# Performance work log

Hardware: AMD Instinct MI355X
Metric: run time of the kernel (lower is better)

The kernel has to match this reference:

```python
import jax, jax.numpy as jnp
import numpy as np
import math

NUM_HEADS = 4
NUM_GROUPS = 16
EPS = 1e-5


def setup_inputs() -> dict:
    key = jax.random.key(0)
    ks = jax.random.split(key, 4)
    C = 256
    x = jax.random.normal(ks[0], (1, C, 16, 16, 16), dtype=jnp.float32)
    gn_gamma = jnp.ones((C,), dtype=jnp.float32)
    gn_beta = jnp.zeros((C,), dtype=jnp.float32)
    # conv3d 1x1 kernels == plain matrices [out_ch, in_ch]
    w_qkv = jax.random.normal(ks[1], (3 * C, C), dtype=jnp.float32) * (1.0 / math.sqrt(C))
    w_proj = jax.random.normal(ks[2], (C, C), dtype=jnp.float32) * (1.0 / math.sqrt(C))
    b_proj = jnp.zeros((C,), dtype=jnp.float32)
    return {"x": x, "gn_gamma": gn_gamma, "gn_beta": gn_beta,
            "w_qkv": w_qkv, "w_proj": w_proj, "b_proj": b_proj}


def reference(x, gn_gamma, gn_beta, w_qkv, w_proj, b_proj):
    B, C, H, W, D = x.shape
    N = H * W * D
    heads = NUM_HEADS
    d = C // heads

    xf = x.reshape(B, C, N)  # [B, C, N]

    # GroupNorm(16, C) with affine params
    xg = xf.reshape(B, NUM_GROUPS, C // NUM_GROUPS, N)
    mu = jnp.mean(xg, axis=(2, 3), keepdims=True)
    var = jnp.var(xg, axis=(2, 3), keepdims=True)
    xn = ((xg - mu) * jax.lax.rsqrt(var + EPS)).reshape(B, C, N)
    xn = xn * gn_gamma[None, :, None] + gn_beta[None, :, None]

    # 1x1 conv QKV: [B, 3C, N]
    qkv = jnp.einsum('oc,bcn->bon', w_qkv, xn)
    # torch: qkv.reshape(B*heads, 3d, N).chunk(3, dim=1)
    qkv = qkv.reshape(B * heads, 3 * d, N)
    q, k, v = qkv[:, :d], qkv[:, d:2 * d], qkv[:, 2 * d:]

    scale = 1.0 / math.sqrt(math.sqrt(d))
    attn = jnp.einsum('bct,bcs->bts', q * scale, k * scale)  # [B*heads, N, N]
    attn = jax.nn.softmax(attn, axis=-1)
    h = jnp.einsum('bts,bcs->bct', attn, v)  # [B*heads, d, N]

    h = h.reshape(B, C, N)
    out = jnp.einsum('oc,bcn->bon', w_proj, h) + b_proj[None, :, None]
    return (out + xf).reshape(B, C, H, W, D)
```

## Files before the change

kernel.cpp:

```cpp
#include <hip/hip_runtime.h>
#include <math.h>

#define N_TOK 4096
#define C_CH  256
#define SPLITS 4

typedef short bf16x8 __attribute__((ext_vector_type(8)));
typedef float f32x4  __attribute__((ext_vector_type(4)));
typedef unsigned short u16;

__device__ __forceinline__ u16 f2bf(float f) {
    union { float f; unsigned u; } v; v.f = f;
    unsigned r = v.u + 0x7FFF + ((v.u >> 16) & 1);
    return (u16)(r >> 16);
}
__device__ __forceinline__ float bf2f(u16 b) {
    union { unsigned u; float f; } v; v.u = ((unsigned)b) << 16;
    return v.f;
}
__device__ __forceinline__ unsigned packtr(float a, float b) {
    union { float f; unsigned u; } ua, ub; ua.f = a; ub.f = b;
    return __builtin_amdgcn_perm(ub.u, ua.u, 0x07060302u);
}

__global__ __launch_bounds__(256) void prep(const float* __restrict__ wqkv,
                                            const float* __restrict__ wproj,
                                            const float* __restrict__ x,
                                            u16* __restrict__ wq, u16* __restrict__ wp,
                                            float2* __restrict__ part) {
    __shared__ float rs[4], rss[4];
    if (blockIdx.x < 1024) {
        int i = blockIdx.x * 256 + threadIdx.x;
        if (i < 196608) {
            int row = i >> 8;
            float s = ((row % 192) < 64) ? 0.125f : 1.0f;
            wq[i] = f2bf(wqkv[i] * s);
        } else {
            wp[i - 196608] = f2bf(wproj[i - 196608]);
        }
    } else {
        const int b = blockIdx.x - 1024, tid = threadIdx.x;
        const int lane = tid & 63, wave = tid >> 6;
        const float4* xp = (const float4*)x + b * 1024;
        float s = 0.f, ss = 0.f;
#pragma unroll
        for (int k = 0; k < 4; ++k) {
            float4 v = xp[tid + k * 256];
            s  += v.x + v.y + v.z + v.w;
            ss += v.x * v.x + v.y * v.y + v.z * v.z + v.w * v.w;
        }
#pragma unroll
        for (int off = 1; off < 64; off <<= 1) {
            s  += __shfl_xor(s, off, 64);
            ss += __shfl_xor(ss, off, 64);
        }
        if (lane == 0) { rs[wave] = s; rss[wave] = ss; }
        __syncthreads();
        if (tid == 0) part[b] = make_float2(rs[0]+rs[1]+rs[2]+rs[3], rss[0]+rss[1]+rss[2]+rss[3]);
    }
}

__global__ __launch_bounds__(256) void norm_t(const float* __restrict__ x,
                                              const float2* __restrict__ part,
                                              const float* __restrict__ gamma,
                                              const float* __restrict__ beta,
                                              u16* __restrict__ xt) {
    const int tb = blockIdx.x * 64, cb = blockIdx.y * 64;
    const int tid = threadIdx.x;
    __shared__ float T[64][65];
    __shared__ float smu[16], srstd[16];
    if (tid < 16) {
        float s = 0.f, ss = 0.f;
#pragma unroll
        for (int j = 0; j < 16; ++j) { float2 p = part[tid * 16 + j]; s += p.x; ss += p.y; }
        float mu = s / 65536.f;
        float var = ss / 65536.f - mu * mu;
        smu[tid] = mu; srstd[tid] = rsqrtf(var + 1e-5f);
    }
    __syncthreads();
#pragma unroll
    for (int it = 0; it < 16; ++it) {
        int idx = tid + it * 256;
        int c = idx >> 6, t = idx & 63;
        int cg = cb + c;
        T[c][t] = (x[cg * N_TOK + tb + t] - smu[cg >> 4]) * srstd[cg >> 4] * gamma[cg] + beta[cg];
    }
    __syncthreads();
#pragma unroll
    for (int it = 0; it < 16; ++it) {
        int idx = tid + it * 256;
        int t = idx >> 6, c = idx & 63;
        xt[(tb + t) * C_CH + cb + c] = f2bf(T[c][t]);
    }
}

__global__ __launch_bounds__(256) void qkv_gemm(const u16* __restrict__ wq,
                                                const u16* __restrict__ xt,
                                                u16* __restrict__ QT,
                                                u16* __restrict__ KTm,
                                                u16* __restrict__ Vc) {
    const int nb = blockIdx.x * 64;
    const int mo = blockIdx.y * 64 + (threadIdx.x >> 6) * 16;
    const int lane = threadIdx.x & 63;
    const int quad = lane >> 4, low = lane & 15;

    f32x4 acc[4] = {f32x4{0,0,0,0}, f32x4{0,0,0,0}, f32x4{0,0,0,0}, f32x4{0,0,0,0}};
#pragma unroll
    for (int kc = 0; kc < 8; ++kc) {
        bf16x8 af = *(const bf16x8*)(wq + (mo + low) * 256 + kc * 32 + quad * 8);
#pragma unroll
        for (int nt = 0; nt < 4; ++nt) {
            bf16x8 bf_ = *(const bf16x8*)(xt + (nb + nt * 16 + low) * 256 + kc * 32 + quad * 8);
            acc[nt] = __builtin_amdgcn_mfma_f32_16x16x32_bf16(af, bf_, acc[nt], 0, 0, 0);
        }
    }
#pragma unroll
    for (int r = 0; r < 4; ++r) {
        int o = mo + quad * 4 + r;
        int head = o / 192, rem = o % 192, c = rem & 63;
#pragma unroll
        for (int nt = 0; nt < 4; ++nt) {
            int tok = nb + nt * 16 + low;
            u16 v = f2bf(acc[nt][r]);
            if (rem < 64)       QT [(head * N_TOK + tok) * 64 + c] = v;
            else if (rem < 128) KTm[(head * N_TOK + tok) * 64 + c] = v;
            else                Vc [(head * 64 + c) * N_TOK + tok] = v;
        }
    }
}

__global__ __launch_bounds__(256, 2) void attn_kernel(const u16* __restrict__ QT,
                                                      const u16* __restrict__ KTm,
                                                      const u16* __restrict__ Vc,
                                                      u16* __restrict__ Op,
                                                      float* __restrict__ Lp) {
    const int head = blockIdx.y, split = blockIdx.z;
    const int qb   = blockIdx.x * 128;
    const int tid  = threadIdx.x;
    const int wave = tid >> 6, lane = tid & 63;
    const int quad = lane >> 4, low = lane & 15;

    const u16* Qh = QT  + head * N_TOK * 64;
    const u16* Kh = KTm + head * N_TOK * 64 + split * 1024 * 64;
    const u16* Vh = Vc  + head * 64 * N_TOK + split * 1024;

    __shared__ u16 Ks[64 * 64];
    __shared__ u16 Vs[64 * 64];
    __shared__ u16 Ps[4 * 32 * 64];
    u16* Pw = Ps + wave * 2048;

    bf16x8 ones;
#pragma unroll
    for (int i = 0; i < 8; ++i) ones[i] = (short)0x3F80;

    bf16x8 bq[2][2];
#pragma unroll
    for (int tn = 0; tn < 2; ++tn)
#pragma unroll
        for (int kh = 0; kh < 2; ++kh)
            bq[tn][kh] = *(const bf16x8*)(Qh + (qb + wave * 32 + tn * 16 + low) * 64 + kh * 32 + quad * 8);

    f32x4 oa[2][4], lC[2];
#pragma unroll
    for (int mt = 0; mt < 2; ++mt) {
        lC[mt] = f32x4{0,0,0,0};
#pragma unroll
        for (int cn = 0; cn < 4; ++cn) oa[mt][cn] = f32x4{0,0,0,0};
    }

    const int sA = tid >> 3, gA = tid & 7;
    const int swA = ((gA ^ (sA & 7)) * 8);
    const int swB = ((gA ^ ((sA + 32) & 7)) * 8);
    uint4 pk0 = *(const uint4*)(Kh + sA * 64 + gA * 8);
    uint4 pk1 = *(const uint4*)(Kh + (sA + 32) * 64 + gA * 8);
    uint4 pv0 = *(const uint4*)(Vh + sA * N_TOK + gA * 8);
    uint4 pv1 = *(const uint4*)(Vh + (sA + 32) * N_TOK + gA * 8);

    const int low7 = low & 7;

    for (int kt = 0; kt < 16; ++kt) {
        __syncthreads();
        *(uint4*)(Ks + sA * 64 + swA) = pk0;
        *(uint4*)(Ks + (sA + 32) * 64 + swB) = pk1;
        *(uint4*)(Vs + sA * 64 + swA) = pv0;
        *(uint4*)(Vs + (sA + 32) * 64 + swB) = pv1;
        if (kt < 15) {
            int sb2 = (kt + 1) * 64;
            pk0 = *(const uint4*)(Kh + (sb2 + sA) * 64 + gA * 8);
            pk1 = *(const uint4*)(Kh + (sb2 + sA + 32) * 64 + gA * 8);
            pv0 = *(const uint4*)(Vh + sA * N_TOK + sb2 + gA * 8);
            pv1 = *(const uint4*)(Vh + (sA + 32) * N_TOK + sb2 + gA * 8);
        }
        __syncthreads();

        f32x4 sa[4][2];
#pragma unroll
        for (int sm = 0; sm < 4; ++sm)
#pragma unroll
            for (int tn = 0; tn < 2; ++tn) sa[sm][tn] = f32x4{0,0,0,0};
#pragma unroll
        for (int kh = 0; kh < 2; ++kh)
#pragma unroll
            for (int sm = 0; sm < 4; ++sm) {
                bf16x8 ak = *(const bf16x8*)(Ks + (sm * 16 + low) * 64 + (((quad + 4 * kh) ^ low7) * 8));
#pragma unroll
                for (int tn = 0; tn < 2; ++tn)
                    sa[sm][tn] = __builtin_amdgcn_mfma_f32_16x16x32_bf16(ak, bq[tn][kh], sa[sm][tn], 0, 0, 0);
            }

#pragma unroll
        for (int sm = 0; sm < 4; ++sm)
#pragma unroll
            for (int tn = 0; tn < 2; ++tn) {
                float p0 = __expf(sa[sm][tn][0]);
                float p1 = __expf(sa[sm][tn][1]);
                float p2 = __expf(sa[sm][tn][2]);
                float p3 = __expf(sa[sm][tn][3]);
                uint2 pk; pk.x = packtr(p0, p1); pk.y = packtr(p2, p3);
                int t = tn * 16 + low;
                int sw = ((sm * 2 + (quad >> 1)) ^ low7);
                *(uint2*)(Pw + t * 64 + sw * 8 + (quad & 1) * 4) = pk;
            }
        asm volatile("s_waitcnt lgkmcnt(0)" ::: "memory");

#pragma unroll
        for (int kh = 0; kh < 2; ++kh) {
            bf16x8 ap0 = *(const bf16x8*)(Pw + (low) * 64      + (((quad + 4 * kh) ^ low7) * 8));
            bf16x8 ap1 = *(const bf16x8*)(Pw + (16 + low) * 64 + (((quad + 4 * kh) ^ low7) * 8));
            lC[0] = __builtin_amdgcn_mfma_f32_16x16x32_bf16(ap0, ones, lC[0], 0, 0, 0);
            lC[1] = __builtin_amdgcn_mfma_f32_16x16x32_bf16(ap1, ones, lC[1], 0, 0, 0);
#pragma unroll
            for (int cn = 0; cn < 4; ++cn) {
                bf16x8 bv = *(const bf16x8*)(Vs + (cn * 16 + low) * 64 + (((quad + 4 * kh) ^ low7) * 8));
                oa[0][cn] = __builtin_amdgcn_mfma_f32_16x16x32_bf16(ap0, bv, oa[0][cn], 0, 0, 0);
                oa[1][cn] = __builtin_amdgcn_mfma_f32_16x16x32_bf16(ap1, bv, oa[1][cn], 0, 0, 0);
            }
        }
    }

    const int sh = (split * 4 + head) * N_TOK;
#pragma unroll
    for (int mt = 0; mt < 2; ++mt)
#pragma unroll
        for (int r = 0; r < 4; ++r) {
            int t = qb + wave * 32 + mt * 16 + quad * 4 + r;
            if (low == 0) Lp[sh + t] = lC[mt][r];
#pragma unroll
            for (int cn = 0; cn < 4; ++cn)
                Op[(sh + t) * 64 + cn * 16 + low] = f2bf(oa[mt][cn][r]);
        }
}

__global__ __launch_bounds__(256) void proj_gemm(const u16* __restrict__ wp,
                                                 const u16* __restrict__ Op,
                                                 const float* __restrict__ Lp,
                                                 const float* __restrict__ bias,
                                                 const float* __restrict__ xres,
                                                 float* __restrict__ out) {
    const int nb = blockIdx.x * 64;
    const int mo = blockIdx.y * 64 + (threadIdx.x >> 6) * 16;
    const int lane = threadIdx.x & 63;
    const int quad = lane >> 4, low = lane & 15;

    __shared__ u16 hT[64 * 264];

#pragma unroll
    for (int i = 0; i < 8; ++i) {
        int idx = i * 256 + threadIdx.x;
        int t = idx >> 5, cc = idx & 31;
        int head = cc >> 3;
        int tok = nb + t;
        float l = 0.f;
        float o[8] = {0.f,0.f,0.f,0.f,0.f,0.f,0.f,0.f};
#pragma unroll
        for (int sp = 0; sp < SPLITS; ++sp) {
            int b = (sp * 4 + head) * N_TOK + tok;
            l += Lp[b];
            uint4 pv = *(const uint4*)(Op + b * 64 + (cc & 7) * 8);
            const u16* ps = (const u16*)&pv;
#pragma unroll
            for (int j = 0; j < 8; ++j) o[j] += bf2f(ps[j]);
        }
        float rl = 1.f / l;
        u16 res[8];
#pragma unroll
        for (int j = 0; j < 8; ++j) res[j] = f2bf(o[j] * rl);
        *(uint4*)(hT + t * 264 + cc * 8) = *(const uint4*)res;
    }
    __syncthreads();

    f32x4 acc[4] = {f32x4{0,0,0,0}, f32x4{0,0,0,0}, f32x4{0,0,0,0}, f32x4{0,0,0,0}};
#pragma unroll
    for (int kc = 0; kc < 8; ++kc) {
        bf16x8 af = *(const bf16x8*)(wp + (mo + low) * 256 + kc * 32 + quad * 8);
#pragma unroll
        for (int nt = 0; nt < 4; ++nt) {
            bf16x8 bf_ = *(const bf16x8*)(hT + (nt * 16 + low) * 264 + kc * 32 + quad * 8);
            acc[nt] = __builtin_amdgcn_mfma_f32_16x16x32_bf16(af, bf_, acc[nt], 0, 0, 0);
        }
    }
#pragma unroll
    for (int r = 0; r < 4; ++r) {
        int o = mo + quad * 4 + r;
        float bv = bias[o];
#pragma unroll
        for (int nt = 0; nt < 4; ++nt) {
            int tok = nb + nt * 16 + low;
            out[o * N_TOK + tok] = acc[nt][r] + bv + xres[o * N_TOK + tok];
        }
    }
}

extern "C" void kernel_launch(void* const* d_in, const int* in_sizes, int n_in,
                              void* d_out, int out_size, void* d_ws, size_t ws_size,
                              hipStream_t stream) {
    const float* x      = (const float*)d_in[0];
    const float* gamma  = (const float*)d_in[1];
    const float* beta   = (const float*)d_in[2];
    const float* w_qkv  = (const float*)d_in[3];
    const float* w_proj = (const float*)d_in[4];
    const float* b_proj = (const float*)d_in[5];
    float* out = (float*)d_out;

    char* base = (char*)d_ws;
    u16*    Op    = (u16*)base;
    u16*    xt    = (u16*)base;
    float*  Lp    = (float*)(base + 8388608);
    float2* part  = (float2*)(base + 8654848);
    u16*    wq    = (u16*)(base + 8658944);
    u16*    wp    = (u16*)(base + 9052160);
    u16*    QT    = (u16*)(base + 9183232);
    u16*    KTm   = (u16*)(base + 11280384);
    u16*    Vc    = (u16*)(base + 13377536);

    prep      <<<1280, 256, 0, stream>>>(w_qkv, w_proj, x, wq, wp, part);
    norm_t    <<<dim3(64, 4),  256, 0, stream>>>(x, part, gamma, beta, xt);
    qkv_gemm  <<<dim3(64, 12), 256, 0, stream>>>(wq, xt, QT, KTm, Vc);
    attn_kernel<<<dim3(32, 4, SPLITS), 256, 0, stream>>>(QT, KTm, Vc, Op, Lp);
    proj_gemm <<<dim3(64, 4),  256, 0, stream>>>(wp, Op, Lp, b_proj, x, out);
}
```

Baseline: 122.8 us.

## Fuse GroupNorm into QKV GEMM, double-buffer attention K/V, use exp2 softmax

Removes the separate normalize/transpose kernel by having each QKV GEMM block normalize its token tile of x into swizzled shared memory, at the cost of recomputing the norm across the 12 output-row blocks. The attention kernel gains double-buffered K/V shared tiles with a single barrier per iteration. It also switches to exp2 by folding log2(e) into the Q weight scale. The projection GEMM is retiled to 32 tokens by 128 output rows per block.

```diff
diff --git a/kernel.cpp b/kernel.cpp
--- a/kernel.cpp
+++ b/kernel.cpp
@@ -33,7 +33,7 @@
         int i = blockIdx.x * 256 + threadIdx.x;
         if (i < 196608) {
             int row = i >> 8;
-            float s = ((row % 192) < 64) ? 0.125f : 1.0f;
+            float s = ((row % 192) < 64) ? 0.18033688f : 1.0f;
             wq[i] = f2bf(wqkv[i] * s);
         } else {
             wp[i - 196608] = f2bf(wproj[i - 196608]);
@@ -60,49 +60,47 @@
     }
 }
 
-__global__ __launch_bounds__(256) void norm_t(const float* __restrict__ x,
-                                              const float2* __restrict__ part,
-                                              const float* __restrict__ gamma,
-                                              const float* __restrict__ beta,
-                                              u16* __restrict__ xt) {
-    const int tb = blockIdx.x * 64, cb = blockIdx.y * 64;
-    const int tid = threadIdx.x;
-    __shared__ float T[64][65];
-    __shared__ float smu[16], srstd[16];
-    if (tid < 16) {
-        float s = 0.f, ss = 0.f;
-#pragma unroll
-        for (int j = 0; j < 16; ++j) { float2 p = part[tid * 16 + j]; s += p.x; ss += p.y; }
-        float mu = s / 65536.f;
-        float var = ss / 65536.f - mu * mu;
-        smu[tid] = mu; srstd[tid] = rsqrtf(var + 1e-5f);
-    }
-    __syncthreads();
-#pragma unroll
-    for (int it = 0; it < 16; ++it) {
-        int idx = tid + it * 256;
-        int c = idx >> 6, t = idx & 63;
-        int cg = cb + c;
-        T[c][t] = (x[cg * N_TOK + tb + t] - smu[cg >> 4]) * srstd[cg >> 4] * gamma[cg] + beta[cg];
-    }
-    __syncthreads();
-#pragma unroll
-    for (int it = 0; it < 16; ++it) {
-        int idx = tid + it * 256;
-        int t = idx >> 6, c = idx & 63;
-        xt[(tb + t) * C_CH + cb + c] = f2bf(T[c][t]);
-    }
-}
-
 __global__ __launch_bounds__(256) void qkv_gemm(const u16* __restrict__ wq,
-                                                const u16* __restrict__ xt,
+                                                const float* __restrict__ x,
+                                                const float2* __restrict__ part,
+                                                const float* __restrict__ gamma,
+                                                const float* __restrict__ beta,
                                                 u16* __restrict__ QT,
                                                 u16* __restrict__ KTm,
                                                 u16* __restrict__ Vc) {
     const int nb = blockIdx.x * 64;
-    const int mo = blockIdx.y * 64 + (threadIdx.x >> 6) * 16;
-    const int lane = threadIdx.x & 63;
+    const int tid = threadIdx.x;
+    const int wave = tid >> 6, lane = tid & 63;
     const int quad = lane >> 4, low = lane & 15;
+    const int mo = blockIdx.y * 64 + wave * 16;
+
+    __shared__ u16 Xs[64 * 256];
+    __shared__ float sca[256], scb[256];
+
+    {
+        const int ch = tid, g = ch >> 4;
+        float s = 0.f, ss = 0.f;
+#pragma unroll
+        for (int j = 0; j < 16; ++j) { float2 p = part[g * 16 + j]; s += p.x; ss += p.y; }
+        float mu = s * (1.f / 65536.f);
+        float var = ss * (1.f / 65536.f) - mu * mu;
+        float a = rsqrtf(var + 1e-5f) * gamma[ch];
+        sca[ch] = a; scb[ch] = beta[ch] - mu * a;
+    }
+    __syncthreads();
+
+#pragma unroll
+    for (int i = 0; i < 8; ++i) {
+        const int g = wave * 8 + i;
+        u16 pk[8];
+#pragma unroll
+        for (int j = 0; j < 8; ++j) {
+            const int ch = g * 8 + j;
+            pk[j] = f2bf(x[ch * N_TOK + nb + lane] * sca[ch] + scb[ch]);
+        }
+        *(uint4*)(Xs + lane * 256 + ((g ^ (lane & 7)) * 8)) = *(const uint4*)pk;
+    }
+    __syncthreads();
 
     f32x4 acc[4] = {f32x4{0,0,0,0}, f32x4{0,0,0,0}, f32x4{0,0,0,0}, f32x4{0,0,0,0}};
 #pragma unroll
@@ -110,7 +108,8 @@
         bf16x8 af = *(const bf16x8*)(wq + (mo + low) * 256 + kc * 32 + quad * 8);
 #pragma unroll
         for (int nt = 0; nt < 4; ++nt) {
-            bf16x8 bf_ = *(const bf16x8*)(xt + (nb + nt * 16 + low) * 256 + kc * 32 + quad * 8);
+            bf16x8 bf_ = *(const bf16x8*)(Xs + (nt * 16 + low) * 256 +
+                                          (((kc * 4 + quad) ^ (low & 7)) * 8));
             acc[nt] = __builtin_amdgcn_mfma_f32_16x16x32_bf16(af, bf_, acc[nt], 0, 0, 0);
         }
     }
@@ -144,8 +143,8 @@
     const u16* Kh = KTm + head * N_TOK * 64 + split * 1024 * 64;
     const u16* Vh = Vc  + head * 64 * N_TOK + split * 1024;
 
-    __shared__ u16 Ks[64 * 64];
-    __shared__ u16 Vs[64 * 64];
+    __shared__ u16 Ks[2][64 * 64];
+    __shared__ u16 Vs[2][64 * 64];
     __shared__ u16 Ps[4 * 32 * 64];
     u16* Pw = Ps + wave * 2048;
 
@@ -175,23 +174,36 @@
     uint4 pk1 = *(const uint4*)(Kh + (sA + 32) * 64 + gA * 8);
     uint4 pv0 = *(const uint4*)(Vh + sA * N_TOK + gA * 8);
     uint4 pv1 = *(const uint4*)(Vh + (sA + 32) * N_TOK + gA * 8);
+    *(uint4*)(Ks[0] + sA * 64 + swA) = pk0;
+    *(uint4*)(Ks[0] + (sA + 32) * 64 + swB) = pk1;
+    *(uint4*)(Vs[0] + sA * 64 + swA) = pv0;
+    *(uint4*)(Vs[0] + (sA + 32) * 64 + swB) = pv1;
+    pk0 = *(const uint4*)(Kh + (64 + sA) * 64 + gA * 8);
+    pk1 = *(const uint4*)(Kh + (64 + sA + 32) * 64 + gA * 8);
+    pv0 = *(const uint4*)(Vh + sA * N_TOK + 64 + gA * 8);
+    pv1 = *(const uint4*)(Vh + (sA + 32) * N_TOK + 64 + gA * 8);
 
     const int low7 = low & 7;
 
     for (int kt = 0; kt < 16; ++kt) {
+        const int cur = kt & 1;
+        const u16* Kc = Ks[cur];
+        const u16* Vu = Vs[cur];
         __syncthreads();
-        *(uint4*)(Ks + sA * 64 + swA) = pk0;
-        *(uint4*)(Ks + (sA + 32) * 64 + swB) = pk1;
-        *(uint4*)(Vs + sA * 64 + swA) = pv0;
-        *(uint4*)(Vs + (sA + 32) * 64 + swB) = pv1;
         if (kt < 15) {
-            int sb2 = (kt + 1) * 64;
-            pk0 = *(const uint4*)(Kh + (sb2 + sA) * 64 + gA * 8);
-            pk1 = *(const uint4*)(Kh + (sb2 + sA + 32) * 64 + gA * 8);
-            pv0 = *(const uint4*)(Vh + sA * N_TOK + sb2 + gA * 8);
-            pv1 = *(const uint4*)(Vh + (sA + 32) * N_TOK + sb2 + gA * 8);
-        }
-        __syncthreads();
+            u16* Kn = Ks[cur ^ 1]; u16* Vn = Vs[cur ^ 1];
+            *(uint4*)(Kn + sA * 64 + swA) = pk0;
+            *(uint4*)(Kn + (sA + 32) * 64 + swB) = pk1;
+            *(uint4*)(Vn + sA * 64 + swA) = pv0;
+            *(uint4*)(Vn + (sA + 32) * 64 + swB) = pv1;
+            if (kt < 14) {
+                int sb2 = (kt + 2) * 64;
+                pk0 = *(const uint4*)(Kh + (sb2 + sA) * 64 + gA * 8);
+                pk1 = *(const uint4*)(Kh + (sb2 + sA + 32) * 64 + gA * 8);
+                pv0 = *(const uint4*)(Vh + sA * N_TOK + sb2 + gA * 8);
+                pv1 = *(const uint4*)(Vh + (sA + 32) * N_TOK + sb2 + gA * 8);
+            }
+        }
 
         f32x4 sa[4][2];
 #pragma unroll
@@ -202,7 +214,7 @@
         for (int kh = 0; kh < 2; ++kh)
 #pragma unroll
             for (int sm = 0; sm < 4; ++sm) {
-                bf16x8 ak = *(const bf16x8*)(Ks + (sm * 16 + low) * 64 + (((quad + 4 * kh) ^ low7) * 8));
+                bf16x8 ak = *(const bf16x8*)(Kc + (sm * 16 + low) * 64 + (((quad + 4 * kh) ^ low7) * 8));
 #pragma unroll
                 for (int tn = 0; tn < 2; ++tn)
                     sa[sm][tn] = __builtin_amdgcn_mfma_f32_16x16x32_bf16(ak, bq[tn][kh], sa[sm][tn], 0, 0, 0);
@@ -212,10 +224,10 @@
         for (int sm = 0; sm < 4; ++sm)
 #pragma unroll
             for (int tn = 0; tn < 2; ++tn) {
-                float p0 = __expf(sa[sm][tn][0]);
-                float p1 = __expf(sa[sm][tn][1]);
-                float p2 = __expf(sa[sm][tn][2]);
-                float p3 = __expf(sa[sm][tn][3]);
+                float p0 = exp2f(sa[sm][tn][0]);
+                float p1 = exp2f(sa[sm][tn][1]);
+                float p2 = exp2f(sa[sm][tn][2]);
+                float p3 = exp2f(sa[sm][tn][3]);
                 uint2 pk; pk.x = packtr(p0, p1); pk.y = packtr(p2, p3);
                 int t = tn * 16 + low;
                 int sw = ((sm * 2 + (quad >> 1)) ^ low7);
@@ -231,7 +243,7 @@
             lC[1] = __builtin_amdgcn_mfma_f32_16x16x32_bf16(ap1, ones, lC[1], 0, 0, 0);
 #pragma unroll
             for (int cn = 0; cn < 4; ++cn) {
-                bf16x8 bv = *(const bf16x8*)(Vs + (cn * 16 + low) * 64 + (((quad + 4 * kh) ^ low7) * 8));
+                bf16x8 bv = *(const bf16x8*)(Vu + (cn * 16 + low) * 64 + (((quad + 4 * kh) ^ low7) * 8));
                 oa[0][cn] = __builtin_amdgcn_mfma_f32_16x16x32_bf16(ap0, bv, oa[0][cn], 0, 0, 0);
                 oa[1][cn] = __builtin_amdgcn_mfma_f32_16x16x32_bf16(ap1, bv, oa[1][cn], 0, 0, 0);
             }
@@ -257,15 +269,15 @@
                                                  const float* __restrict__ bias,
                                                  const float* __restrict__ xres,
                                                  float* __restrict__ out) {
-    const int nb = blockIdx.x * 64;
-    const int mo = blockIdx.y * 64 + (threadIdx.x >> 6) * 16;
+    const int nb = blockIdx.x * 32;
+    const int mo = blockIdx.y * 128 + (threadIdx.x >> 6) * 32;
     const int lane = threadIdx.x & 63;
     const int quad = lane >> 4, low = lane & 15;
 
-    __shared__ u16 hT[64 * 264];
-
-#pragma unroll
-    for (int i = 0; i < 8; ++i) {
+    __shared__ u16 hT[32 * 264];
+
+#pragma unroll
+    for (int i = 0; i < 4; ++i) {
         int idx = i * 256 + threadIdx.x;
         int t = idx >> 5, cc = idx & 31;
         int head = cc >> 3;
@@ -289,26 +301,31 @@
     }
     __syncthreads();
 
-    f32x4 acc[4] = {f32x4{0,0,0,0}, f32x4{0,0,0,0}, f32x4{0,0,0,0}, f32x4{0,0,0,0}};
+    f32x4 acc[2][2] = {{f32x4{0,0,0,0}, f32x4{0,0,0,0}}, {f32x4{0,0,0,0}, f32x4{0,0,0,0}}};
 #pragma unroll
     for (int kc = 0; kc < 8; ++kc) {
-        bf16x8 af = *(const bf16x8*)(wp + (mo + low) * 256 + kc * 32 + quad * 8);
-#pragma unroll
-        for (int nt = 0; nt < 4; ++nt) {
-            bf16x8 bf_ = *(const bf16x8*)(hT + (nt * 16 + low) * 264 + kc * 32 + quad * 8);
-            acc[nt] = __builtin_amdgcn_mfma_f32_16x16x32_bf16(af, bf_, acc[nt], 0, 0, 0);
-        }
-    }
-#pragma unroll
-    for (int r = 0; r < 4; ++r) {
-        int o = mo + quad * 4 + r;
-        float bv = bias[o];
-#pragma unroll
-        for (int nt = 0; nt < 4; ++nt) {
-            int tok = nb + nt * 16 + low;
-            out[o * N_TOK + tok] = acc[nt][r] + bv + xres[o * N_TOK + tok];
-        }
-    }
+#pragma unroll
+        for (int mt = 0; mt < 2; ++mt) {
+            bf16x8 af = *(const bf16x8*)(wp + (mo + mt * 16 + low) * 256 + kc * 32 + quad * 8);
+#pragma unroll
+            for (int nt = 0; nt < 2; ++nt) {
+                bf16x8 bf_ = *(const bf16x8*)(hT + (nt * 16 + low) * 264 + kc * 32 + quad * 8);
+                acc[mt][nt] = __builtin_amdgcn_mfma_f32_16x16x32_bf16(af, bf_, acc[mt][nt], 0, 0, 0);
+            }
+        }
+    }
+#pragma unroll
+    for (int mt = 0; mt < 2; ++mt)
+#pragma unroll
+        for (int r = 0; r < 4; ++r) {
+            int o = mo + mt * 16 + quad * 4 + r;
+            float bv = bias[o];
+#pragma unroll
+            for (int nt = 0; nt < 2; ++nt) {
+                int tok = nb + nt * 16 + low;
+                out[o * N_TOK + tok] = acc[mt][nt][r] + bv + xres[o * N_TOK + tok];
+            }
+        }
 }
 
 extern "C" void kernel_launch(void* const* d_in, const int* in_sizes, int n_in,
@@ -324,7 +341,6 @@
 
     char* base = (char*)d_ws;
     u16*    Op    = (u16*)base;
-    u16*    xt    = (u16*)base;
     float*  Lp    = (float*)(base + 8388608);
     float2* part  = (float2*)(base + 8654848);
     u16*    wq    = (u16*)(base + 8658944);
@@ -334,8 +350,7 @@
     u16*    Vc    = (u16*)(base + 13377536);
 
     prep      <<<1280, 256, 0, stream>>>(w_qkv, w_proj, x, wq, wp, part);
-    norm_t    <<<dim3(64, 4),  256, 0, stream>>>(x, part, gamma, beta, xt);
-    qkv_gemm  <<<dim3(64, 12), 256, 0, stream>>>(wq, xt, QT, KTm, Vc);
+    qkv_gemm  <<<dim3(64, 12), 256, 0, stream>>>(wq, x, part, gamma, beta, QT, KTm, Vc);
     attn_kernel<<<dim3(32, 4, SPLITS), 256, 0, stream>>>(QT, KTm, Vc, Op, Lp);
-    proj_gemm <<<dim3(64, 4),  256, 0, stream>>>(wp, Op, Lp, b_proj, x, out);
-}
+    proj_gemm <<<dim3(128, 2), 256, 0, stream>>>(wp, Op, Lp, b_proj, x, out);
+}
```

Result: no change. 122.1 us (-0.6%).
